# Kernel tuning notes

Measured on AMD Instinct MI355X. Metric: run time of the kernel, lower is better.

## Reference

```python
import jax, jax.numpy as jnp
import numpy as np

B, C, H, W = 64, 512, 8, 8
K = 100            # num_class
H1, HID, L = 64, 128, 32   # ae_hidden[0], fixed hidd, ae_latent
CLIP = 100.0       # CSSRClassifier.clip_len
RED = -0.1         # model='pcssr' -> -1, times gamma=0.1
PUSH_THRESH = 10000.0


def setup_inputs() -> dict:
    key = jax.random.key(0)
    ks = jax.random.split(key, 9)
    s = lambda fan_in: 1.0 / np.sqrt(fan_in)  # kaiming-ish 1x1 conv init scale
    return {
        "x": jax.random.normal(ks[0], (B, C, H, W), jnp.float32),
        "ycls": jax.random.randint(ks[1], (B,), 0, K),
        "safe_margin_all": jax.random.normal(ks[2], (K,), jnp.float32),
        "safe_distance_all": jax.random.normal(ks[3], (K,), jnp.float32),
        "W1": jax.random.normal(ks[4], (K, H1, C), jnp.float32) * s(C),
        "W2": jax.random.normal(ks[5], (K, HID, H1), jnp.float32) * s(H1),
        "W3": jax.random.normal(ks[6], (K, L, HID), jnp.float32) * s(HID),
        "prototypes": jax.random.normal(ks[7], (K, L, H, W), jnp.float32),
        "prototypes1": jax.random.normal(ks[8], (K, L, H, W), jnp.float32),
    }


def reference(x, ycls, safe_margin_all, safe_distance_all, W1, W2, W3, prototypes, prototypes1):
    P = H * W
    xf = x.reshape(B, C, P)
    # per-class 1x1-conv encoder (tanh after every conv), batched over classes k
    h = jnp.tanh(jnp.einsum('koc,bcp->kbop', W1, xf))      # [K,B,H1,P]
    h = jnp.tanh(jnp.einsum('koi,kbip->kbop', W2, h))      # [K,B,HID,P]
    lt = jnp.tanh(jnp.einsum('koi,kbip->kbop', W3, h))     # [K,B,L,P]
    p = prototypes.reshape(K, 1, L, P)
    p1 = prototypes1.reshape(K, 1, L, P)
    # squared-L2 distance over channel dim, scaled by reduction, clipped
    er = jnp.clip(jnp.sum((lt - p) ** 2, axis=2) * RED, -CLIP, CLIP)    # [K,B,P]
    er1 = jnp.clip(jnp.sum((lt - p1) ** 2, axis=2) * RED, -CLIP, CLIP)  # [K,B,P]
    # training losses (pull on er1, push on er), vectorized across classes
    f = jnp.sum(er, axis=2)    # [K,B] spatial-summed errors
    f1 = jnp.sum(er1, axis=2)  # [K,B]
    cls_ids = jnp.arange(K)[:, None]
    mask_eq = (ycls[None, :] == cls_ids).astype(f.dtype)   # [K,B]
    n_eq = jnp.sum(mask_eq, axis=1)
    pull = jnp.sum(jnp.where(n_eq > 0,
                             jnp.sum(f1 * mask_eq, axis=1) / jnp.maximum(n_eq, 1.0),
                             0.0))
    comb = (1.0 - mask_eq) * (f < PUSH_THRESH).astype(f.dtype)
    n_comb = jnp.sum(comb, axis=1)
    push = jnp.sum(jnp.where(n_comb > 0,
                             jnp.sum(f * comb, axis=1) / jnp.maximum(n_comb, 1.0),
                             0.0))
    # cat per-class [B,1,H,W] errors along dim 1 -> [B,K,H,W]
    logits = jnp.transpose(er, (1, 0, 2)).reshape(B, K, H, W)
    logits1 = jnp.transpose(er1, (1, 0, 2)).reshape(B, K, H, W)
    return logits, logits1, pull, push
```

## Files before the change

### kernel.cpp

```cpp
#include <hip/hip_runtime.h>

typedef short  s16x8  __attribute__((ext_vector_type(8)));
typedef float  f32x16 __attribute__((ext_vector_type(16)));
typedef unsigned short u16;
typedef unsigned int   u32;
typedef unsigned long long u64b;

#define MFMA32(a,b,c) __builtin_amdgcn_mfma_f32_32x32x16_bf16((a),(b),(c),0,0,0)
#define KCLS 100

__device__ __forceinline__ u16 f2bf(float f) {
  return (u16)(__builtin_bit_cast(unsigned, f) >> 16);
}

__device__ __forceinline__ u32 pk2bf(float lo, float hi) {
  return (__builtin_bit_cast(u32, lo) >> 16) | (__builtin_bit_cast(u32, hi) & 0xffff0000u);
}

__device__ __forceinline__ float tanh_fast(float x) {
  float e = __builtin_amdgcn_exp2f(x * 2.8853900817779268f);
  return 1.0f - 2.0f * __builtin_amdgcn_rcpf(e + 1.0f);
}

__global__ void prep(const float* __restrict__ x, const float* __restrict__ w1,
                     const float* __restrict__ w2, const float* __restrict__ w3,
                     u16* __restrict__ xF, u16* __restrict__ W1F,
                     u16* __restrict__ W2F, u16* __restrict__ W3F,
                     float* __restrict__ fz, float* __restrict__ out2) {
  __shared__ float tile[64][65];
  const int bid = blockIdx.x, t = threadIdx.x;
  if (bid == 0 && t < 2) out2[t] = 0.f;
  if (bid < 512) {
    const int b = bid >> 3, ck = bid & 7;
    #pragma unroll
    for (int j = 0; j < 4; j++) {
      int e4 = j * 1024 + t * 4;
      int c = e4 >> 6, p0 = e4 & 63;
      float4 v = *(const float4*)(x + ((size_t)b * 512 + ck * 64 + c) * 64 + p0);
      tile[c][p0] = v.x; tile[c][p0 + 1] = v.y; tile[c][p0 + 2] = v.z; tile[c][p0 + 3] = v.w;
    }
    __syncthreads();
    #pragma unroll
    for (int i = 0; i < 2; i++) {
      int s = i * 256 + t;
      int ksl = s >> 7, ph = (s >> 6) & 1, lane = s & 63;
      int cb = ksl * 16 + (lane >> 5) * 8, pp = ph * 32 + (lane & 31);
      u16 o[8];
      #pragma unroll
      for (int jj = 0; jj < 8; jj++) o[jj] = f2bf(tile[cb + jj][pp]);
      *(uint4*)(xF + (((size_t)b * 64 + (ck * 4 + ksl) * 2 + ph) * 512) + lane * 8) = *(uint4*)o;
    }
  } else if (bid < 1312) {
    int base = (bid - 512) * 512;
    #pragma unroll
    for (int i = 0; i < 2; i++) {
      int s = base + i * 256 + t;
      int frag = s >> 6, lane = s & 63;
      int k = frag >> 6, fr = frag & 63;
      int m = (fr & 1) * 32 + (lane & 31);
      int c0 = (fr >> 1) * 16 + (lane >> 5) * 8;
      const float* src = w1 + ((size_t)k * 64 + m) * 512 + c0;
      float4 a = *(const float4*)src, b4 = *(const float4*)(src + 4);
      u16 o[8] = { f2bf(a.x), f2bf(a.y), f2bf(a.z), f2bf(a.w),
                   f2bf(b4.x), f2bf(b4.y), f2bf(b4.z), f2bf(b4.w) };
      *(uint4*)(W1F + ((size_t)frag * 512) + lane * 8) = *(uint4*)o;
    }
  } else if (bid < 1512) {
    int base = (bid - 1312) * 512;
    #pragma unroll
    for (int i = 0; i < 2; i++) {
      int s = base + i * 256 + t;
      int frag = s >> 6, lane = s & 63;
      int k = frag >> 4, fr = frag & 15;
      int m = (fr & 3) * 32 + (lane & 31);
      int c0 = (fr >> 2) * 16 + (lane >> 5) * 8;
      const float* src = w2 + ((size_t)k * 128 + m) * 64 + c0;
      float4 a = *(const float4*)src, b4 = *(const float4*)(src + 4);
      u16 o[8] = { f2bf(a.x), f2bf(a.y), f2bf(a.z), f2bf(a.w),
                   f2bf(b4.x), f2bf(b4.y), f2bf(b4.z), f2bf(b4.w) };
      *(uint4*)(W2F + ((size_t)frag * 512) + lane * 8) = *(uint4*)o;
    }
  } else if (bid < 1612) {
    int base = (bid - 1512) * 512;
    #pragma unroll
    for (int i = 0; i < 2; i++) {
      int s = base + i * 256 + t;
      int frag = s >> 6, lane = s & 63;
      int k = frag >> 3, kb = frag & 7;
      int m = lane & 31;
      int c0 = kb * 16 + (lane >> 5) * 8;
      const float* src = w3 + ((size_t)k * 32 + m) * 128 + c0;
      float4 a = *(const float4*)src, b4 = *(const float4*)(src + 4);
      u16 o[8] = { f2bf(a.x), f2bf(a.y), f2bf(a.z), f2bf(a.w),
                   f2bf(b4.x), f2bf(b4.y), f2bf(b4.z), f2bf(b4.w) };
      *(uint4*)(W3F + ((size_t)frag * 512) + lane * 8) = *(uint4*)o;
    }
  } else {
    int i4 = (bid - 1612) * 256 + t;
    if (i4 < 3200) {
      float4 z = {0.f, 0.f, 0.f, 0.f};
      *(float4*)(fz + (size_t)i4 * 4) = z;
    }
  }
}

template<int GG>
__device__ __forceinline__ s16x8 mk_bfrag(const f32x16 a) {
  u32 P0 = pk2bf(tanh_fast(a[8 * GG + 0]), tanh_fast(a[8 * GG + 1]));
  u32 P1 = pk2bf(tanh_fast(a[8 * GG + 2]), tanh_fast(a[8 * GG + 3]));
  u32 Q0 = pk2bf(tanh_fast(a[8 * GG + 4]), tanh_fast(a[8 * GG + 5]));
  u32 Q1 = pk2bf(tanh_fast(a[8 * GG + 6]), tanh_fast(a[8 * GG + 7]));
  asm("v_permlane32_swap_b32 %0, %1" : "+v"(P0), "+v"(Q0));
  asm("v_permlane32_swap_b32 %0, %1" : "+v"(P1), "+v"(Q1));
  int4 wv = { (int)P0, (int)P1, (int)Q0, (int)Q1 };
  return __builtin_bit_cast(s16x8, wv);
}

__global__ __launch_bounds__(256, 4) void cssr_main(
    const u16* __restrict__ W1F, const u16* __restrict__ W2F, const u16* __restrict__ W3F,
    const u16* __restrict__ xF, const float* __restrict__ protos,
    const float* __restrict__ protos1, float* __restrict__ out,
    float* __restrict__ fw, float* __restrict__ f1w)
{
  const int bid = blockIdx.x;
  const int k = bid >> 5, bp = bid & 31;
  const int tid = threadIdx.x, w = tid >> 6, lane = tid & 63;
  const int bq = w >> 1, ph = w & 1;
  const int b = bp * 2 + bq;
  const int h = lane >> 5, nn = lane & 31;

  const u16* xb  = xF  + ((size_t)b * 64) * 512 + lane * 8;
  const u16* Wk1 = W1F + ((size_t)k * 64) * 512 + lane * 8;

  f32x16 acc1[2] = {};
  #pragma unroll
  for (int ksl = 0; ksl < 32; ksl++) {
    s16x8 B  = *(const s16x8*)(xb  + (ksl * 2 + ph) * 512);
    s16x8 A0 = *(const s16x8*)(Wk1 + (ksl * 2 + 0) * 512);
    s16x8 A1 = *(const s16x8*)(Wk1 + (ksl * 2 + 1) * 512);
    acc1[0] = MFMA32(A0, B, acc1[0]);
    acc1[1] = MFMA32(A1, B, acc1[1]);
  }

  s16x8 b1[4];
  b1[0] = mk_bfrag<0>(acc1[0]); b1[1] = mk_bfrag<1>(acc1[0]);
  b1[2] = mk_bfrag<0>(acc1[1]); b1[3] = mk_bfrag<1>(acc1[1]);

  const u16* Wk2 = W2F + ((size_t)k * 16) * 512 + lane * 8;
  f32x16 acc2[4] = {};
  #pragma unroll
  for (int kb = 0; kb < 4; kb++) {
    #pragma unroll
    for (int m4 = 0; m4 < 4; m4++) {
      s16x8 A = *(const s16x8*)(Wk2 + (kb * 4 + m4) * 512);
      acc2[m4] = MFMA32(A, b1[kb], acc2[m4]);
    }
  }

  s16x8 b2[8];
  b2[0] = mk_bfrag<0>(acc2[0]); b2[1] = mk_bfrag<1>(acc2[0]);
  b2[2] = mk_bfrag<0>(acc2[1]); b2[3] = mk_bfrag<1>(acc2[1]);
  b2[4] = mk_bfrag<0>(acc2[2]); b2[5] = mk_bfrag<1>(acc2[2]);
  b2[6] = mk_bfrag<0>(acc2[3]); b2[7] = mk_bfrag<1>(acc2[3]);

  const u16* Wk3 = W3F + ((size_t)k * 8) * 512 + lane * 8;
  f32x16 acc3 = {};
  #pragma unroll
  for (int kb = 0; kb < 8; kb++) {
    s16x8 A = *(const s16x8*)(Wk3 + kb * 512);
    acc3 = MFMA32(A, b2[kb], acc3);
  }

  const int p = ph * 32 + nn;
  const float* pr  = protos  + (size_t)k * 2048 + p;
  const float* pr1 = protos1 + (size_t)k * 2048 + p;
  float d2 = 0.f, d21 = 0.f;
  #pragma unroll
  for (int g = 0; g < 4; g++) {
    #pragma unroll
    for (int q = 0; q < 4; q++) {
      int m = q + 8 * g + 4 * h;
      float lt = tanh_fast(acc3[g * 4 + q]);
      float d = lt - pr [m * 64];  d2  += d * d;
      float e = lt - pr1[m * 64];  d21 += e * e;
    }
  }
  d2 += __shfl_xor(d2, 32); d21 += __shfl_xor(d21, 32);
  float er  = fminf(fmaxf(d2  * -0.1f, -100.f), 100.f);
  float er1 = fminf(fmaxf(d21 * -0.1f, -100.f), 100.f);
  if (h == 0) {
    out[(size_t)b * 6400 + k * 64 + p]          = er;
    out[409600 + (size_t)b * 6400 + k * 64 + p] = er1;
  }
  float s = er, s1 = er1;
  s += __shfl_xor(s, 1);  s1 += __shfl_xor(s1, 1);
  s += __shfl_xor(s, 2);  s1 += __shfl_xor(s1, 2);
  s += __shfl_xor(s, 4);  s1 += __shfl_xor(s1, 4);
  s += __shfl_xor(s, 8);  s1 += __shfl_xor(s1, 8);
  s += __shfl_xor(s, 16); s1 += __shfl_xor(s1, 16);
  if (lane == 0) {
    atomicAdd(&fw [k * 64 + b], s);
    atomicAdd(&f1w[k * 64 + b], s1);
  }
}

__global__ void finalize(const float* __restrict__ f, const float* __restrict__ f1,
                         const int* __restrict__ ycls, float* __restrict__ out2) {
  const int k = blockIdx.x, b = threadIdx.x;
  float fv = f[k * 64 + b], f1v = f1[k * 64 + b];
  bool eq = (ycls[b] == k);
  bool cb = (!eq) && (fv < 10000.f);
  float s1 = eq ? f1v : 0.f, ne = eq ? 1.f : 0.f;
  float s  = cb ? fv  : 0.f, nc = cb ? 1.f : 0.f;
  #pragma unroll
  for (int o = 1; o < 64; o <<= 1) {
    s1 += __shfl_xor(s1, o); ne += __shfl_xor(ne, o);
    s  += __shfl_xor(s,  o); nc += __shfl_xor(nc, o);
  }
  if (b == 0) {
    if (ne > 0.f) atomicAdd(&out2[0], s1 / ne);
    if (nc > 0.f) atomicAdd(&out2[1], s / nc);
  }
}

extern "C" void kernel_launch(void* const* d_in, const int* in_sizes, int n_in,
                              void* d_out, int out_size, void* d_ws, size_t ws_size,
                              hipStream_t stream) {
  const float* x     = (const float*)d_in[0];
  const int*   ycls  = (const int*)d_in[1];
  const float* W1    = (const float*)d_in[4];
  const float* W2    = (const float*)d_in[5];
  const float* W3    = (const float*)d_in[6];
  const float* prot  = (const float*)d_in[7];
  const float* prot1 = (const float*)d_in[8];
  float* out = (float*)d_out;

  char* ws = (char*)d_ws;
  u16*  xFb = (u16*)(ws);
  u16*  W1F = (u16*)(ws + 4194304);
  u16*  W2F = (u16*)(ws + 10747904);
  u16*  W3F = (u16*)(ws + 12386304);
  float* fw  = (float*)(ws + 13205504);
  float* f1w = (float*)(ws + 13231104);

  prep<<<1625, 256, 0, stream>>>(x, W1, W2, W3, xFb, W1F, W2F, W3F,
                                 fw, out + 819200);
  cssr_main<<<KCLS * 32, 256, 0, stream>>>(W1F, W2F, W3F, xFb, prot, prot1,
                                           out, fw, f1w);
  finalize<<<KCLS, 64, 0, stream>>>(fw, f1w, ycls, out + 819200);
}
```

Baseline: 150.7 us.

## Stage encoder operands through double-buffered LDS with async global-to-LDS loads

Replaces the per-wave direct global loads of W1/x fragments with cooperative global_load_lds copies into a double-buffered shared pool, so the four waves share one W1 tile and the loads overlap the layer-1 MFMAs. W2 and W3 weights are prefetched into LDS during the tail of the previous layer, and the prototype loads are hoisted ahead of the layer-3 MFMAs. This removes redundant global traffic (each wave previously reloaded W1) and hides load latency. In exchange it adds barriers, manual vmcnt waits, and 48KB of LDS, with launch bounds lowered to 3 blocks per SIMD, which reduces occupancy.

```diff
diff --git a/kernel.cpp b/kernel.cpp
--- a/kernel.cpp
+++ b/kernel.cpp
@@ -8,6 +8,9 @@
 
 #define MFMA32(a,b,c) __builtin_amdgcn_mfma_f32_32x32x16_bf16((a),(b),(c),0,0,0)
 #define KCLS 100
+#define VMCNT(n) asm volatile("s_waitcnt vmcnt(" #n ")" ::: "memory")
+#define BAR()    __builtin_amdgcn_s_barrier()
+#define SCHEDB() __builtin_amdgcn_sched_barrier(0)
 
 __device__ __forceinline__ u16 f2bf(float f) {
   return (u16)(__builtin_bit_cast(unsigned, f) >> 16);
@@ -20,6 +23,12 @@
 __device__ __forceinline__ float tanh_fast(float x) {
   float e = __builtin_amdgcn_exp2f(x * 2.8853900817779268f);
   return 1.0f - 2.0f * __builtin_amdgcn_rcpf(e + 1.0f);
+}
+
+__device__ __forceinline__ void ld_lds16(const void* g, void* l) {
+  __builtin_amdgcn_global_load_lds(
+      (const __attribute__((address_space(1))) unsigned char*)g,
+      (__attribute__((address_space(3))) unsigned char*)l, 16, 0, 0);
 }
 
 __global__ void prep(const float* __restrict__ x, const float* __restrict__ w1,
@@ -116,43 +125,87 @@
   return __builtin_bit_cast(s16x8, wv);
 }
 
-__global__ __launch_bounds__(256, 4) void cssr_main(
+__global__ __launch_bounds__(256, 3) void cssr_main(
     const u16* __restrict__ W1F, const u16* __restrict__ W2F, const u16* __restrict__ W3F,
     const u16* __restrict__ xF, const float* __restrict__ protos,
     const float* __restrict__ protos1, float* __restrict__ out,
     float* __restrict__ fw, float* __restrict__ f1w)
 {
+  __shared__ u16 pool[2][12288];
   const int bid = blockIdx.x;
-  const int k = bid >> 5, bp = bid & 31;
+  const int k = bid >> 5, bpair = bid & 31;
   const int tid = threadIdx.x, w = tid >> 6, lane = tid & 63;
   const int bq = w >> 1, ph = w & 1;
-  const int b = bp * 2 + bq;
+  const int b = bpair * 2 + bq;
   const int h = lane >> 5, nn = lane & 31;
 
-  const u16* xb  = xF  + ((size_t)b * 64) * 512 + lane * 8;
-  const u16* Wk1 = W1F + ((size_t)k * 64) * 512 + lane * 8;
+  const u16* sp[6];
+  int dfo[6];
+  #pragma unroll
+  for (int i = 0; i < 6; i++) {
+    int f = w * 6 + i;
+    dfo[i] = f * 512;
+    if (f < 8) {
+      int ksl = f >> 1, mt = f & 1;
+      sp[i] = W1F + ((size_t)k * 64 + ksl * 2 + mt) * 512 + lane * 8;
+    } else {
+      int g = f - 8, wv = g >> 2, ksl = g & 3;
+      int bs = bpair * 2 + (wv >> 1), ps = wv & 1;
+      sp[i] = xF + ((size_t)bs * 64 + ksl * 2 + ps) * 512 + lane * 8;
+    }
+  }
+
+  #pragma unroll
+  for (int i = 0; i < 6; i++) { ld_lds16(sp[i], &pool[0][dfo[i]]); sp[i] += 4096; }
+  VMCNT(0); BAR();
 
   f32x16 acc1[2] = {};
   #pragma unroll
-  for (int ksl = 0; ksl < 32; ksl++) {
-    s16x8 B  = *(const s16x8*)(xb  + (ksl * 2 + ph) * 512);
-    s16x8 A0 = *(const s16x8*)(Wk1 + (ksl * 2 + 0) * 512);
-    s16x8 A1 = *(const s16x8*)(Wk1 + (ksl * 2 + 1) * 512);
-    acc1[0] = MFMA32(A0, B, acc1[0]);
-    acc1[1] = MFMA32(A1, B, acc1[1]);
+  for (int ci = 0; ci < 8; ci++) {
+    const int cb = ci & 1;
+    if (ci < 7) {
+      #pragma unroll
+      for (int i = 0; i < 6; i++) { ld_lds16(sp[i], &pool[cb ^ 1][dfo[i]]); sp[i] += 4096; }
+      VMCNT(6);
+    } else {
+      #pragma unroll
+      for (int j = 0; j < 4; j++) {
+        int f = w * 4 + j;
+        ld_lds16(W2F + ((size_t)k * 16 + f) * 512 + lane * 8, &pool[0][f * 512]);
+      }
+      VMCNT(4);
+    }
+    BAR(); SCHEDB();
+    const u16* bu = pool[cb];
+    #pragma unroll
+    for (int ksl = 0; ksl < 4; ksl++) {
+      s16x8 A0 = *(const s16x8*)(bu + (ksl * 2 + 0) * 512 + lane * 8);
+      s16x8 A1 = *(const s16x8*)(bu + (ksl * 2 + 1) * 512 + lane * 8);
+      s16x8 B  = *(const s16x8*)(bu + (8 + w * 4 + ksl) * 512 + lane * 8);
+      acc1[0] = MFMA32(A0, B, acc1[0]);
+      acc1[1] = MFMA32(A1, B, acc1[1]);
+    }
+    BAR();
+  }
+
+  #pragma unroll
+  for (int j = 0; j < 2; j++) {
+    int f = w * 2 + j;
+    ld_lds16(W3F + ((size_t)k * 8 + f) * 512 + lane * 8, &pool[1][f * 512]);
   }
 
   s16x8 b1[4];
   b1[0] = mk_bfrag<0>(acc1[0]); b1[1] = mk_bfrag<1>(acc1[0]);
   b1[2] = mk_bfrag<0>(acc1[1]); b1[3] = mk_bfrag<1>(acc1[1]);
 
-  const u16* Wk2 = W2F + ((size_t)k * 16) * 512 + lane * 8;
+  VMCNT(2); BAR(); SCHEDB();
+
   f32x16 acc2[4] = {};
   #pragma unroll
   for (int kb = 0; kb < 4; kb++) {
     #pragma unroll
     for (int m4 = 0; m4 < 4; m4++) {
-      s16x8 A = *(const s16x8*)(Wk2 + (kb * 4 + m4) * 512);
+      s16x8 A = *(const s16x8*)(&pool[0][(kb * 4 + m4) * 512] + lane * 8);
       acc2[m4] = MFMA32(A, b1[kb], acc2[m4]);
     }
   }
@@ -163,26 +216,37 @@
   b2[4] = mk_bfrag<0>(acc2[2]); b2[5] = mk_bfrag<1>(acc2[2]);
   b2[6] = mk_bfrag<0>(acc2[3]); b2[7] = mk_bfrag<1>(acc2[3]);
 
-  const u16* Wk3 = W3F + ((size_t)k * 8) * 512 + lane * 8;
-  f32x16 acc3 = {};
-  #pragma unroll
-  for (int kb = 0; kb < 8; kb++) {
-    s16x8 A = *(const s16x8*)(Wk3 + kb * 512);
-    acc3 = MFMA32(A, b2[kb], acc3);
-  }
+  VMCNT(0); BAR(); SCHEDB();
 
   const int p = ph * 32 + nn;
   const float* pr  = protos  + (size_t)k * 2048 + p;
   const float* pr1 = protos1 + (size_t)k * 2048 + p;
-  float d2 = 0.f, d21 = 0.f;
+  float prv[16], pr1v[16];
   #pragma unroll
   for (int g = 0; g < 4; g++) {
     #pragma unroll
     for (int q = 0; q < 4; q++) {
       int m = q + 8 * g + 4 * h;
+      prv [g * 4 + q] = pr [m * 64];
+      pr1v[g * 4 + q] = pr1[m * 64];
+    }
+  }
+
+  f32x16 acc3 = {};
+  #pragma unroll
+  for (int kb = 0; kb < 8; kb++) {
+    s16x8 A = *(const s16x8*)(&pool[1][kb * 512] + lane * 8);
+    acc3 = MFMA32(A, b2[kb], acc3);
+  }
+
+  float d2 = 0.f, d21 = 0.f;
+  #pragma unroll
+  for (int g = 0; g < 4; g++) {
+    #pragma unroll
+    for (int q = 0; q < 4; q++) {
       float lt = tanh_fast(acc3[g * 4 + q]);
-      float d = lt - pr [m * 64];  d2  += d * d;
-      float e = lt - pr1[m * 64];  d21 += e * e;
+      float d = lt - prv [g * 4 + q];  d2  += d * d;
+      float e = lt - pr1v[g * 4 + q];  d21 += e * e;
     }
   }
   d2 += __shfl_xor(d2, 32); d21 += __shfl_xor(d21, 32);
```

Measured after the change: 144.9 us. 1.04x faster.
